# Optimization experiments

Hardware: AMD Instinct MI355X
Metric: run time of the kernel (lower is better)

Reference implementation:

```python
import jax, jax.numpy as jnp
import numpy as np

B, S, D, H = 2, 2048, 2048, 16
DK = D // H
THETA = 10000.0


def setup_inputs() -> dict:
    key = jax.random.key(0)
    ks = jax.random.split(key, 5)
    scale = 0.02
    return {
        "x": jax.random.normal(ks[0], (B, S, D), dtype=jnp.float32),
        "W_Q": jax.random.normal(ks[1], (D, D), dtype=jnp.float32) * scale,
        "W_K": jax.random.normal(ks[2], (D, D), dtype=jnp.float32) * scale,
        "W_V": jax.random.normal(ks[3], (D, D), dtype=jnp.float32) * scale,
        "W_O": jax.random.normal(ks[4], (D, D), dtype=jnp.float32) * scale,
        "token_positions": jnp.arange(S, dtype=jnp.int32),
    }


def _rope(x, pos):
    # x: [B, S, H, DK]; pos: [S]. Interleaved-pair rotation (cs336 RoPE).
    half = DK // 2
    inv_freq = THETA ** (-(jnp.arange(half, dtype=jnp.float32) / half))  # [half]
    ang = pos.astype(jnp.float32)[:, None] * inv_freq[None, :]           # [S, half]
    cos = jnp.cos(ang)[None, :, None, :]                                 # [1,S,1,half]
    sin = jnp.sin(ang)[None, :, None, :]
    x1, x2 = x[..., ::2], x[..., 1::2]
    r1 = x1 * cos - x2 * sin
    r2 = x1 * sin + x2 * cos
    return jnp.stack([r1, r2], axis=-1).reshape(x.shape)


def reference(x, W_Q, W_K, W_V, W_O, token_positions):
    # QKV projections (Linear with no bias: y = x @ W^T)
    Q = (x @ W_Q.T).reshape(B, S, H, DK)
    K = (x @ W_K.T).reshape(B, S, H, DK)
    V = (x @ W_V.T).reshape(B, S, H, DK)
    Q = _rope(Q, token_positions)
    K = _rope(K, token_positions)
    scores = jnp.einsum("bqhd,bkhd->bhqk", Q, K) / jnp.sqrt(jnp.float32(DK))
    causal = jnp.tril(jnp.ones((S, S), dtype=bool))  # True = attend
    scores = jnp.where(causal[None, None], scores, -jnp.inf)
    attn = jax.nn.softmax(scores, axis=-1)
    out = jnp.einsum("bhqk,bkhd->bqhd", attn, V).reshape(B, S, D)
    return out @ W_O.T
```

## Files before the change

### kernel.cpp

```cpp
#include <hip/hip_runtime.h>
#include <hip/hip_bf16.h>
#include <cstdint>
#include <cstddef>

#define B_ 2
#define S_ 2048
#define D_ 2048
#define H_ 16
#define DK_ 128
#define M_ (B_*S_)

typedef __attribute__((ext_vector_type(8))) __bf16 bf16x8;
typedef __attribute__((ext_vector_type(4))) float f32x4;
typedef __attribute__((ext_vector_type(16))) float f32x16;

__device__ __forceinline__ unsigned short f2bf(float f) {
  union { float f; unsigned int u; } v; v.f = f;
  unsigned int r = (v.u + 0x7fffu + ((v.u >> 16) & 1u)) >> 16;
  return (unsigned short)r;
}
__device__ __forceinline__ float bf2f(unsigned short b) {
  union { unsigned int u; float f; } v; v.u = ((unsigned int)b) << 16;
  return v.f;
}

__device__ __forceinline__ void gld16(const void* g, void* l) {
  __builtin_amdgcn_global_load_lds(
      (const __attribute__((address_space(1))) unsigned int*)g,
      (__attribute__((address_space(3))) unsigned int*)l, 16, 0, 0);
}

__global__ void cvt_all(const float* __restrict__ x,  const float* __restrict__ Wq,
                        const float* __restrict__ Wk, const float* __restrict__ Wv,
                        const float* __restrict__ Wo, unsigned short* __restrict__ dst) {
  size_t i = ((size_t)blockIdx.x * blockDim.x + threadIdx.x) * 4;
  const float* src;
  size_t off;
  if (i < ((size_t)M_ * D_)) {
    src = x; off = i;
  } else {
    size_t j = i - (size_t)M_ * D_;
    int w = (int)(j >> 22);
    off = j & ((1u << 22) - 1);
    src = (w == 0) ? Wq : (w == 1) ? Wk : (w == 2) ? Wv : Wo;
  }
  float4 v = *(const float4*)(src + off);
  dst[i+0] = f2bf(v.x); dst[i+1] = f2bf(v.y);
  dst[i+2] = f2bf(v.z); dst[i+3] = f2bf(v.w);
}

template<int WRITE_BF16>
__global__ __launch_bounds__(512, 2) void gemm8p(const unsigned short* __restrict__ A,
                                                 const unsigned short* __restrict__ W0,
                                                 const unsigned short* __restrict__ W1,
                                                 const unsigned short* __restrict__ W2,
                                                 void* __restrict__ C0, void* __restrict__ C1,
                                                 void* __restrict__ C2,
                                                 int M, int N, int K) {
  __shared__ unsigned short sA[2][2][256 * 32];
  __shared__ unsigned short sB[2][2][256 * 32];
  const int z = blockIdx.z;
  const unsigned short* Bt = (z == 0) ? W0 : (z == 1) ? W1 : W2;
  void* Cout = (z == 0) ? C0 : (z == 1) ? C1 : C2;

  const int tid  = threadIdx.x;
  const int lane = tid & 63;
  const int wid  = tid >> 6;
  const int wm = wid >> 2, wn = wid & 3;
  const int l16 = lane & 15, quad = lane >> 4;
  const int col16 = quad ^ ((lane >> 1) & 3);
  const int qk_log = (lane & 3) ^ ((lane >> 3) & 3);
  const int srow = lane >> 2;
  const int bm = blockIdx.y * 256, bn = blockIdx.x * 256;
  const int NT = K >> 6;

  f32x4 acc[8][4];
  #pragma unroll
  for (int i = 0; i < 8; ++i)
    #pragma unroll
    for (int j = 0; j < 4; ++j)
      acc[i][j] = (f32x4){0.f, 0.f, 0.f, 0.f};

  auto stage = [&](const unsigned short* __restrict__ g, int rowbase,
                   unsigned short* l, int t, int kh) {
    const unsigned short* src = g + (size_t)rowbase * K + t * 64 + kh * 32 + qk_log * 8;
    #pragma unroll
    for (int p = 0; p < 2; ++p) {
      const int i = wid * 2 + p;
      gld16(src + (size_t)(i * 16 + srow) * K, l + i * 512);
    }
  };

  stage(A,  bm, &sA[0][0][0], 0, 0);
  stage(Bt, bn, &sB[0][0][0], 0, 0);
  stage(A,  bm, &sA[0][1][0], 0, 1);
  stage(Bt, bn, &sB[0][1][0], 0, 1);
  stage(A,  bm, &sA[1][0][0], 1, 0);
  stage(Bt, bn, &sB[1][0][0], 1, 0);
  asm volatile("s_waitcnt vmcnt(4)" ::: "memory");
  __builtin_amdgcn_s_barrier();

  for (int t = 0; t < NT; ++t) {
    const int buf = t & 1;
    bf16x8 bfrag[4];
    #pragma unroll
    for (int ph = 0; ph < 4; ++ph) {
      const int ks = ph >> 1;
      const int mh = ph & 1;
      bf16x8 afrag[4];
      const unsigned short* aP = &sA[buf][ks][0] +
          (size_t)((wm * 128 + mh * 64 + l16) * 4 + col16) * 8;
      #pragma unroll
      for (int mf = 0; mf < 4; ++mf)
        afrag[mf] = *(const bf16x8*)(aP + mf * 512);
      if (mh == 0) {
        const unsigned short* bP = &sB[buf][ks][0] +
            (size_t)((wn * 64 + l16) * 4 + col16) * 8;
        #pragma unroll
        for (int nf = 0; nf < 4; ++nf)
          bfrag[nf] = *(const bf16x8*)(bP + nf * 512);
      }
      if (ph == 0)      { if (t + 1 < NT) stage(A,  bm, &sA[buf ^ 1][1][0], t + 1, 1); }
      else if (ph == 1) { if (t + 1 < NT) stage(Bt, bn, &sB[buf ^ 1][1][0], t + 1, 1); }
      else if (ph == 2) { if (t + 2 < NT) stage(A,  bm, &sA[buf][0][0],     t + 2, 0); }
      else              { if (t + 2 < NT) stage(Bt, bn, &sB[buf][0][0],     t + 2, 0); }

      __builtin_amdgcn_s_barrier();
      asm volatile("s_waitcnt lgkmcnt(0)" ::: "memory");
      __builtin_amdgcn_s_setprio(1);
      #pragma unroll
      for (int nf = 0; nf < 4; ++nf)
        #pragma unroll
        for (int mf = 0; mf < 4; ++mf)
          acc[mh * 4 + mf][nf] = __builtin_amdgcn_mfma_f32_16x16x32_bf16(
              afrag[mf], bfrag[nf], acc[mh * 4 + mf][nf], 0, 0, 0);
      __builtin_amdgcn_s_setprio(0);
      if (ph == 3) {
        if (t + 2 < NT) asm volatile("s_waitcnt vmcnt(4)" ::: "memory");
        else            asm volatile("s_waitcnt vmcnt(0)" ::: "memory");
      }
      __builtin_amdgcn_s_barrier();
    }
  }

  #pragma unroll
  for (int mf = 0; mf < 8; ++mf) {
    const int row = bm + wm * 128 + mf * 16 + quad * 4;
    #pragma unroll
    for (int nf = 0; nf < 4; ++nf) {
      const int col = bn + wn * 64 + nf * 16 + l16;
      #pragma unroll
      for (int r = 0; r < 4; ++r) {
        if (WRITE_BF16)
          ((unsigned short*)Cout)[(size_t)(row + r) * N + col] = f2bf(acc[mf][nf][r]);
        else
          ((float*)Cout)[(size_t)(row + r) * N + col] = acc[mf][nf][r];
      }
    }
  }
}

template<int WRITE_BF16>
__global__ __launch_bounds__(256) void gemm_bt(const unsigned short* __restrict__ A,
                                               const unsigned short* __restrict__ W0,
                                               const unsigned short* __restrict__ W1,
                                               const unsigned short* __restrict__ W2,
                                               void* __restrict__ C0, void* __restrict__ C1,
                                               void* __restrict__ C2,
                                               int M, int N, int K) {
  __shared__ unsigned short sA[128 * 32];
  __shared__ unsigned short sB[128 * 32];
  const int z = blockIdx.z;
  const unsigned short* Bt = (z == 0) ? W0 : (z == 1) ? W1 : W2;
  void* Cout = (z == 0) ? C0 : (z == 1) ? C1 : C2;

  const int tid  = threadIdx.x;
  const int lane = tid & 63;
  const int wid  = tid >> 6;
  const int wm = wid >> 1, wn = wid & 1;
  const int quad = lane >> 4, l16 = lane & 15;
  const int bm = blockIdx.y * 128, bn = blockIdx.x * 128;
  const int srow = lane >> 2;
  const int scol = (lane & 3) * 8;

  f32x4 acc[4][4];
  #pragma unroll
  for (int i = 0; i < 4; ++i)
    #pragma unroll
    for (int j = 0; j < 4; ++j)
      acc[i][j] = (f32x4){0.f, 0.f, 0.f, 0.f};

  for (int k0 = 0; k0 < K; k0 += 32) {
    __syncthreads();
    #pragma unroll
    for (int p = 0; p < 2; ++p) {
      int row = p * 64 + wid * 16;
      gld16(A  + (size_t)(bm + row + srow) * K + k0 + scol, sA + row * 32);
      gld16(Bt + (size_t)(bn + row + srow) * K + k0 + scol, sB + row * 32);
    }
    __syncthreads();

    bf16x8 af[4], bfr[4];
    #pragma unroll
    for (int i = 0; i < 4; ++i)
      af[i] = *(const bf16x8*)(sA + (wm * 64 + i * 16 + l16) * 32 + quad * 8);
    #pragma unroll
    for (int j = 0; j < 4; ++j)
      bfr[j] = *(const bf16x8*)(sB + (wn * 64 + j * 16 + l16) * 32 + quad * 8);
    #pragma unroll
    for (int i = 0; i < 4; ++i)
      #pragma unroll
      for (int j = 0; j < 4; ++j)
        acc[i][j] = __builtin_amdgcn_mfma_f32_16x16x32_bf16(af[i], bfr[j], acc[i][j], 0, 0, 0);
  }

  #pragma unroll
  for (int i = 0; i < 4; ++i) {
    int row = bm + wm * 64 + i * 16 + quad * 4;
    #pragma unroll
    for (int j = 0; j < 4; ++j) {
      int col = bn + wn * 64 + j * 16 + l16;
      #pragma unroll
      for (int r = 0; r < 4; ++r) {
        if (WRITE_BF16)
          ((unsigned short*)Cout)[(size_t)(row + r) * N + col] = f2bf(acc[i][j][r]);
        else
          ((float*)Cout)[(size_t)(row + r) * N + col] = acc[i][j][r];
      }
    }
  }
}

__global__ void rope_kernel(unsigned short* __restrict__ Q, unsigned short* __restrict__ K,
                            const int* __restrict__ pos) {
  int idx = blockIdx.x * blockDim.x + threadIdx.x;
  int i = idx & 63;
  int h = (idx >> 6) & (H_ - 1);
  int s = (idx >> 10) & (S_ - 1);
  int b = idx >> 21;
  float p = (float)pos[s];
  float inv = expf(-(float)i * (9.210340371976184f / 64.0f));
  float ang = p * inv;
  float sn, cs;
  sincosf(ang, &sn, &cs);
  size_t base = (((size_t)b * S_ + s) * D_) + (size_t)h * DK_ + 2 * i;
  float x1 = bf2f(Q[base]), x2 = bf2f(Q[base + 1]);
  Q[base]     = f2bf(x1 * cs - x2 * sn);
  Q[base + 1] = f2bf(x1 * sn + x2 * cs);
  x1 = bf2f(K[base]); x2 = bf2f(K[base + 1]);
  K[base]     = f2bf(x1 * cs - x2 * sn);
  K[base + 1] = f2bf(x1 * sn + x2 * cs);
}

__global__ __launch_bounds__(256) void transpose_bf16(const unsigned short* __restrict__ src,
                                                      unsigned short* __restrict__ dst) {
  __shared__ unsigned short sT[64 * 64];
  const int b = blockIdx.y;
  const int tx = blockIdx.x & 31, ty = blockIdx.x >> 5;
  const size_t base = (size_t)b * 2048 * 2048;
  const int m0 = ty * 64, c0 = tx * 64;
  const int tid = threadIdx.x;
  #pragma unroll
  for (int c = 0; c < 2; ++c) {
    int idx = tid + c * 256;
    int row = idx >> 3;
    int chk = idx & 7;
    uint4 v = *(const uint4*)(src + base + (size_t)(m0 + row) * 2048 + c0 + chk * 8);
    *(uint4*)(sT + row * 64 + ((chk ^ (row & 7)) * 8)) = v;
  }
  __syncthreads();
  #pragma unroll
  for (int c = 0; c < 2; ++c) {
    int idx = tid + c * 256;
    int orow = idx >> 3;
    int ocol = (idx & 7) * 8;
    unsigned short tmp[8];
    #pragma unroll
    for (int j = 0; j < 8; ++j) {
      int lr = ocol + j;
      int lc = orow;
      tmp[j] = sT[lr * 64 + (((lc >> 3) ^ (lr & 7)) * 8) + (lc & 7)];
    }
    *(uint4*)(dst + base + (size_t)(c0 + orow) * 2048 + m0 + ocol) = *(const uint4*)tmp;
  }
}

__global__ __launch_bounds__(256, 2) void flash_attn(const unsigned short* __restrict__ Q,
                                                     const unsigned short* __restrict__ K,
                                                     const unsigned short* __restrict__ VT,
                                                     unsigned short* __restrict__ O) {
  __shared__ unsigned short sK[2][64 * 128];
  __shared__ unsigned short sVT[2][128 * 64];
  __shared__ unsigned short sP[4][32 * 64];

  const int tid = threadIdx.x, lane = tid & 63, wid = tid >> 6;
  const int half = lane >> 5, l32 = lane & 31;
  const int qi = 15 - (blockIdx.x & 15);
  const int bh = blockIdx.x >> 4;
  const int h = bh & (H_ - 1), b = bh >> 4;
  const int qw = qi * 128 + wid * 32;
  const size_t qkbase = ((size_t)b * S_) * D_ + (size_t)h * DK_;
  const unsigned short* Qg = Q + qkbase;
  const unsigned short* Kg = K + qkbase;
  const unsigned short* VTg = VT + (size_t)bh * DK_ * S_;
  unsigned short* Og = O + qkbase;
  unsigned short* sPw = sP[wid];

  const int kKeySub = lane >> 4;
  const int kPhys   = lane & 15;
  const int vFeatSub = lane >> 3;
  const int vPhys    = lane & 7;

  bf16x8 qf[8];
  #pragma unroll
  for (int ks = 0; ks < 8; ++ks)
    qf[ks] = *(const bf16x8*)(Qg + (size_t)(qw + l32) * D_ + ks * 16 + half * 8);

  union { unsigned short u[8]; bf16x8 v; } onesu;
  #pragma unroll
  for (int j2 = 0; j2 < 8; ++j2) onesu.u[j2] = 0x3F80;
  const bf16x8 ones = onesu.v;

  f32x16 Oacc[4];
  #pragma unroll
  for (int ft = 0; ft < 4; ++ft)
    #pragma unroll
    for (int r = 0; r < 16; ++r) Oacc[ft][r] = 0.f;
  f32x16 l_acc;
  #pragma unroll
  for (int r = 0; r < 16; ++r) l_acc[r] = 0.f;
  const float scale = 0.08838834764831845f;

  const int nkb = 2 * (qi + 1);

  auto stage = [&](int kb) {
    const int k0 = kb * 64;
    unsigned short* bK = sK[kb & 1];
    unsigned short* bV = sVT[kb & 1];
    #pragma unroll
    for (int p = 0; p < 4; ++p) {
      int issue = wid * 4 + p;
      int key = issue * 4 + kKeySub;
      int logiK = (kPhys & 8) | ((kPhys ^ key) & 7);
      gld16(Kg + (size_t)(k0 + key) * D_ + logiK * 8, bK + issue * 512);
      int feat = issue * 8 + vFeatSub;
      int logiV = vPhys ^ (feat & 7);
      gld16(VTg + (size_t)feat * S_ + k0 + logiV * 8, bV + issue * 512);
    }
  };

  stage(0);

  for (int kb = 0; kb < nkb; ++kb) {
    __syncthreads();
    if (kb + 1 < nkb) stage(kb + 1);

    const int k0 = kb * 64;
    if (k0 > qw + 31) continue;

    const unsigned short* bK = sK[kb & 1];
    const unsigned short* bV = sVT[kb & 1];

    f32x16 sc[2];
    #pragma unroll
    for (int t = 0; t < 2; ++t)
      #pragma unroll
      for (int r = 0; r < 16; ++r) sc[t][r] = 0.f;
    #pragma unroll
    for (int ks = 0; ks < 8; ++ks) {
      const int logi = ks * 2 + half;
      #pragma unroll
      for (int t = 0; t < 2; ++t) {
        const int key = t * 32 + l32;
        const int phys = (logi & 8) | ((logi ^ key) & 7);
        bf16x8 kf = *(const bf16x8*)(bK + key * 128 + phys * 8);
        sc[t] = __builtin_amdgcn_mfma_f32_32x32x16_bf16(qf[ks], kf, sc[t], 0, 0, 0);
      }
    }

    const bool diag = (k0 + 63 > qw);
    #pragma unroll
    for (int t = 0; t < 2; ++t) {
      const int col = t * 32 + l32;
      const int keyg = k0 + col;
      #pragma unroll
      for (int r = 0; r < 16; ++r) {
        const int rl = (r & 3) + 8 * (r >> 2) + 4 * half;
        float v = sc[t][r] * scale;
        if (diag && (keyg > qw + rl)) v = -1e30f;
        sPw[rl * 64 + (((col >> 3) ^ (rl & 7)) * 8) + (col & 7)] = f2bf(__expf(v));
      }
    }

    #pragma unroll
    for (int ksp = 0; ksp < 4; ++ksp) {
      const int logi = ksp * 2 + half;
      bf16x8 pf = *(const bf16x8*)(sPw + l32 * 64 + ((logi ^ (l32 & 7)) * 8));
      l_acc = __builtin_amdgcn_mfma_f32_32x32x16_bf16(pf, ones, l_acc, 0, 0, 0);
      #pragma unroll
      for (int ft = 0; ft < 4; ++ft) {
        const int feat = ft * 32 + l32;
        const int phys = logi ^ (feat & 7);
        bf16x8 vf = *(const bf16x8*)(bV + feat * 64 + phys * 8);
        Oacc[ft] = __builtin_amdgcn_mfma_f32_32x32x16_bf16(pf, vf, Oacc[ft], 0, 0, 0);
      }
    }
  }

  #pragma unroll
  for (int ft = 0; ft < 4; ++ft) {
    const int feat = ft * 32 + l32;
    #pragma unroll
    for (int r = 0; r < 16; ++r) {
      const int rl = (r & 3) + 8 * (r >> 2) + 4 * half;
      Og[(size_t)(qw + rl) * D_ + feat] = f2bf(Oacc[ft][r] / l_acc[r]);
    }
  }
}

extern "C" void kernel_launch(void* const* d_in, const int* in_sizes, int n_in,
                              void* d_out, int out_size, void* d_ws, size_t ws_size,
                              hipStream_t stream) {
  const float* x  = (const float*)d_in[0];
  const float* Wq = (const float*)d_in[1];
  const float* Wk = (const float*)d_in[2];
  const float* Wv = (const float*)d_in[3];
  const float* Wo = (const float*)d_in[4];
  const int*  pos = (const int*)d_in[5];
  float* out = (float*)d_out;

  char* ws = (char*)d_ws;
  size_t off = 0;
  auto alloc = [&](size_t bytes) { void* p = ws + off; off += (bytes + 255) & ~255ULL; return p; };
  const size_t nx = (size_t)M_ * D_;
  const size_t nw = (size_t)D_ * D_;
  unsigned short* xb  = (unsigned short*)alloc(nx * 2);
  unsigned short* wqb = (unsigned short*)alloc(nw * 2);
  unsigned short* wkb = (unsigned short*)alloc(nw * 2);
  unsigned short* wvb = (unsigned short*)alloc(nw * 2);
  unsigned short* wob = (unsigned short*)alloc(nw * 2);
  unsigned short* Qb  = (unsigned short*)alloc(nx * 2);
  unsigned short* Kb  = (unsigned short*)alloc(nx * 2);
  unsigned short* Vb  = (unsigned short*)alloc(nx * 2);
  unsigned short* AOb = xb;
  unsigned short* VTb = wqb;

  hipLaunchKernelGGL(cvt_all, dim3((nx + 4 * nw) / 1024), dim3(256), 0, stream,
                     x, Wq, Wk, Wv, Wo, xb);

  hipLaunchKernelGGL((gemm8p<1>), dim3(D_ / 256, M_ / 256, 3), dim3(512), 0, stream,
                     xb, wqb, wkb, wvb, (void*)Qb, (void*)Kb, (void*)Vb, M_, D_, D_);

  hipLaunchKernelGGL(rope_kernel, dim3((B_ * S_ * H_ * 64) / 256), dim3(256), 0, stream, Qb, Kb, pos);

  hipLaunchKernelGGL(transpose_bf16, dim3(1024, 2), dim3(256), 0, stream, Vb, VTb);

  hipLaunchKernelGGL(flash_attn, dim3(B_ * H_ * (S_ / 128)), dim3(256), 0, stream, Qb, Kb, VTb, AOb);

  hipLaunchKernelGGL((gemm_bt<0>), dim3(D_ / 128, M_ / 128, 1), dim3(256), 0, stream,
                     AOb, wob, wob, wob, (void*)out, (void*)out, (void*)out, M_, D_, D_);
}
```

Measured before the change: 438.5 us.

## Rebalance QKV GEMM grid with smaller V tiles, vectorize RoPE, prioritize attention MFMA

The 3-way QKV GEMM grid of 384 blocks of 256x256 tiles is replaced by a 1D grid of 512 blocks. Q and K keep 256x256 tiles, while V uses 128x256 tiles so the grid spreads better across the 256 CUs and the tail wave shrinks. The RoPE kernel now uses fast intrinsics and packed 32-bit loads and stores. The flash attention MFMA sections are also wrapped in s_setprio. The V tiles have lower arithmetic intensity, and the fast sincos may lose some precision at large angles.

```diff
diff --git a/kernel.cpp b/kernel.cpp
--- a/kernel.cpp
+++ b/kernel.cpp
@@ -49,112 +49,194 @@
   dst[i+2] = f2bf(v.z); dst[i+3] = f2bf(v.w);
 }
 
-template<int WRITE_BF16>
-__global__ __launch_bounds__(512, 2) void gemm8p(const unsigned short* __restrict__ A,
-                                                 const unsigned short* __restrict__ W0,
-                                                 const unsigned short* __restrict__ W1,
-                                                 const unsigned short* __restrict__ W2,
-                                                 void* __restrict__ C0, void* __restrict__ C1,
-                                                 void* __restrict__ C2,
-                                                 int M, int N, int K) {
+__global__ __launch_bounds__(512, 2) void gemm_qkv(const unsigned short* __restrict__ A,
+                                                   const unsigned short* __restrict__ W0,
+                                                   const unsigned short* __restrict__ W1,
+                                                   const unsigned short* __restrict__ W2,
+                                                   unsigned short* __restrict__ C0,
+                                                   unsigned short* __restrict__ C1,
+                                                   unsigned short* __restrict__ C2,
+                                                   int M, int N, int K) {
   __shared__ unsigned short sA[2][2][256 * 32];
   __shared__ unsigned short sB[2][2][256 * 32];
-  const int z = blockIdx.z;
-  const unsigned short* Bt = (z == 0) ? W0 : (z == 1) ? W1 : W2;
-  void* Cout = (z == 0) ? C0 : (z == 1) ? C1 : C2;
-
+  const int id   = blockIdx.x;
   const int tid  = threadIdx.x;
   const int lane = tid & 63;
   const int wid  = tid >> 6;
-  const int wm = wid >> 2, wn = wid & 3;
   const int l16 = lane & 15, quad = lane >> 4;
   const int col16 = quad ^ ((lane >> 1) & 3);
   const int qk_log = (lane & 3) ^ ((lane >> 3) & 3);
   const int srow = lane >> 2;
-  const int bm = blockIdx.y * 256, bn = blockIdx.x * 256;
   const int NT = K >> 6;
 
-  f32x4 acc[8][4];
-  #pragma unroll
-  for (int i = 0; i < 8; ++i)
-    #pragma unroll
-    for (int j = 0; j < 4; ++j)
-      acc[i][j] = (f32x4){0.f, 0.f, 0.f, 0.f};
-
-  auto stage = [&](const unsigned short* __restrict__ g, int rowbase,
-                   unsigned short* l, int t, int kh) {
-    const unsigned short* src = g + (size_t)rowbase * K + t * 64 + kh * 32 + qk_log * 8;
-    #pragma unroll
-    for (int p = 0; p < 2; ++p) {
-      const int i = wid * 2 + p;
-      gld16(src + (size_t)(i * 16 + srow) * K, l + i * 512);
-    }
-  };
-
-  stage(A,  bm, &sA[0][0][0], 0, 0);
-  stage(Bt, bn, &sB[0][0][0], 0, 0);
-  stage(A,  bm, &sA[0][1][0], 0, 1);
-  stage(Bt, bn, &sB[0][1][0], 0, 1);
-  stage(A,  bm, &sA[1][0][0], 1, 0);
-  stage(Bt, bn, &sB[1][0][0], 1, 0);
-  asm volatile("s_waitcnt vmcnt(4)" ::: "memory");
-  __builtin_amdgcn_s_barrier();
-
-  for (int t = 0; t < NT; ++t) {
-    const int buf = t & 1;
-    bf16x8 bfrag[4];
-    #pragma unroll
-    for (int ph = 0; ph < 4; ++ph) {
-      const int ks = ph >> 1;
-      const int mh = ph & 1;
-      bf16x8 afrag[4];
-      const unsigned short* aP = &sA[buf][ks][0] +
-          (size_t)((wm * 128 + mh * 64 + l16) * 4 + col16) * 8;
-      #pragma unroll
-      for (int mf = 0; mf < 4; ++mf)
-        afrag[mf] = *(const bf16x8*)(aP + mf * 512);
-      if (mh == 0) {
-        const unsigned short* bP = &sB[buf][ks][0] +
+  if (id < 256) {
+    const int z = id >> 7, r = id & 127;
+    const unsigned short* Bt = z ? W1 : W0;
+    unsigned short* Cout = z ? C1 : C0;
+    const int bm = (r >> 3) * 256, bn = (r & 7) * 256;
+    const int wm = wid >> 2, wn = wid & 3;
+
+    f32x4 acc[8][4];
+    #pragma unroll
+    for (int i = 0; i < 8; ++i)
+      #pragma unroll
+      for (int j = 0; j < 4; ++j)
+        acc[i][j] = (f32x4){0.f, 0.f, 0.f, 0.f};
+
+    auto stage = [&](const unsigned short* __restrict__ g, int rowbase,
+                     unsigned short* l, int t, int kh) {
+      const unsigned short* src = g + (size_t)rowbase * K + t * 64 + kh * 32 + qk_log * 8;
+      #pragma unroll
+      for (int p = 0; p < 2; ++p) {
+        const int i = wid * 2 + p;
+        gld16(src + (size_t)(i * 16 + srow) * K, l + i * 512);
+      }
+    };
+
+    stage(A,  bm, &sA[0][0][0], 0, 0);
+    stage(Bt, bn, &sB[0][0][0], 0, 0);
+    stage(A,  bm, &sA[0][1][0], 0, 1);
+    stage(Bt, bn, &sB[0][1][0], 0, 1);
+    stage(A,  bm, &sA[1][0][0], 1, 0);
+    stage(Bt, bn, &sB[1][0][0], 1, 0);
+    asm volatile("s_waitcnt vmcnt(4)" ::: "memory");
+    __builtin_amdgcn_s_barrier();
+
+    for (int t = 0; t < NT; ++t) {
+      const int buf = t & 1;
+      bf16x8 bfrag[4];
+      #pragma unroll
+      for (int ph = 0; ph < 4; ++ph) {
+        const int ks = ph >> 1;
+        const int mh = ph & 1;
+        bf16x8 afrag[4];
+        const unsigned short* aP = &sA[buf][ks][0] +
+            (size_t)((wm * 128 + mh * 64 + l16) * 4 + col16) * 8;
+        #pragma unroll
+        for (int mf = 0; mf < 4; ++mf)
+          afrag[mf] = *(const bf16x8*)(aP + mf * 512);
+        if (mh == 0) {
+          const unsigned short* bP = &sB[buf][ks][0] +
+              (size_t)((wn * 64 + l16) * 4 + col16) * 8;
+          #pragma unroll
+          for (int nf = 0; nf < 4; ++nf)
+            bfrag[nf] = *(const bf16x8*)(bP + nf * 512);
+        }
+        if (ph == 0)      { if (t + 1 < NT) stage(A,  bm, &sA[buf ^ 1][1][0], t + 1, 1); }
+        else if (ph == 1) { if (t + 1 < NT) stage(Bt, bn, &sB[buf ^ 1][1][0], t + 1, 1); }
+        else if (ph == 2) { if (t + 2 < NT) stage(A,  bm, &sA[buf][0][0],     t + 2, 0); }
+        else              { if (t + 2 < NT) stage(Bt, bn, &sB[buf][0][0],     t + 2, 0); }
+
+        __builtin_amdgcn_s_barrier();
+        asm volatile("s_waitcnt lgkmcnt(0)" ::: "memory");
+        __builtin_amdgcn_s_setprio(1);
+        #pragma unroll
+        for (int nf = 0; nf < 4; ++nf)
+          #pragma unroll
+          for (int mf = 0; mf < 4; ++mf)
+            acc[mh * 4 + mf][nf] = __builtin_amdgcn_mfma_f32_16x16x32_bf16(
+                afrag[mf], bfrag[nf], acc[mh * 4 + mf][nf], 0, 0, 0);
+        __builtin_amdgcn_s_setprio(0);
+        if (ph == 3) {
+          if (t + 2 < NT) asm volatile("s_waitcnt vmcnt(4)" ::: "memory");
+          else            asm volatile("s_waitcnt vmcnt(0)" ::: "memory");
+        }
+        __builtin_amdgcn_s_barrier();
+      }
+    }
+
+    #pragma unroll
+    for (int mf = 0; mf < 8; ++mf) {
+      const int row = bm + wm * 128 + mf * 16 + quad * 4;
+      #pragma unroll
+      for (int nf = 0; nf < 4; ++nf) {
+        const int col = bn + wn * 64 + nf * 16 + l16;
+        #pragma unroll
+        for (int rr = 0; rr < 4; ++rr)
+          Cout[(size_t)(row + rr) * N + col] = f2bf(acc[mf][nf][rr]);
+      }
+    }
+  } else {
+    const int r = id - 256;
+    const unsigned short* Bt = W2;
+    unsigned short* Cout = C2;
+    const int bm = (r >> 3) * 128, bn = (r & 7) * 256;
+    const int wm = wid >> 2, wn = wid & 3;
+
+    f32x4 acc[4][4];
+    #pragma unroll
+    for (int i = 0; i < 4; ++i)
+      #pragma unroll
+      for (int j = 0; j < 4; ++j)
+        acc[i][j] = (f32x4){0.f, 0.f, 0.f, 0.f};
+
+    auto stageB = [&](unsigned short* l, int t, int kh) {
+      const unsigned short* src = Bt + (size_t)bn * K + t * 64 + kh * 32 + qk_log * 8;
+      #pragma unroll
+      for (int p = 0; p < 2; ++p) {
+        const int i = wid * 2 + p;
+        gld16(src + (size_t)(i * 16 + srow) * K, l + i * 512);
+      }
+    };
+    auto stageA = [&](unsigned short* l, int t, int kh) {
+      const unsigned short* src = A + (size_t)bm * K + t * 64 + kh * 32 + qk_log * 8;
+      gld16(src + (size_t)(wid * 16 + srow) * K, l + wid * 512);
+    };
+
+    stageA(&sA[0][0][0], 0, 0); stageB(&sB[0][0][0], 0, 0);
+    stageA(&sA[0][1][0], 0, 1); stageB(&sB[0][1][0], 0, 1);
+    stageA(&sA[1][0][0], 1, 0); stageB(&sB[1][0][0], 1, 0);
+    asm volatile("s_waitcnt vmcnt(3)" ::: "memory");
+    __builtin_amdgcn_s_barrier();
+
+    for (int t = 0; t < NT; ++t) {
+      const int buf = t & 1;
+      #pragma unroll
+      for (int ph = 0; ph < 2; ++ph) {
+        bf16x8 afrag[4], bfrag[4];
+        const unsigned short* aP = &sA[buf][ph][0] +
+            (size_t)((wm * 64 + l16) * 4 + col16) * 8;
+        #pragma unroll
+        for (int mf = 0; mf < 4; ++mf)
+          afrag[mf] = *(const bf16x8*)(aP + mf * 512);
+        const unsigned short* bP = &sB[buf][ph][0] +
             (size_t)((wn * 64 + l16) * 4 + col16) * 8;
         #pragma unroll
         for (int nf = 0; nf < 4; ++nf)
           bfrag[nf] = *(const bf16x8*)(bP + nf * 512);
-      }
-      if (ph == 0)      { if (t + 1 < NT) stage(A,  bm, &sA[buf ^ 1][1][0], t + 1, 1); }
-      else if (ph == 1) { if (t + 1 < NT) stage(Bt, bn, &sB[buf ^ 1][1][0], t + 1, 1); }
-      else if (ph == 2) { if (t + 2 < NT) stage(A,  bm, &sA[buf][0][0],     t + 2, 0); }
-      else              { if (t + 2 < NT) stage(Bt, bn, &sB[buf][0][0],     t + 2, 0); }
-
-      __builtin_amdgcn_s_barrier();
-      asm volatile("s_waitcnt lgkmcnt(0)" ::: "memory");
-      __builtin_amdgcn_s_setprio(1);
-      #pragma unroll
-      for (int nf = 0; nf < 4; ++nf)
-        #pragma unroll
-        for (int mf = 0; mf < 4; ++mf)
-          acc[mh * 4 + mf][nf] = __builtin_amdgcn_mfma_f32_16x16x32_bf16(
-              afrag[mf], bfrag[nf], acc[mh * 4 + mf][nf], 0, 0, 0);
-      __builtin_amdgcn_s_setprio(0);
-      if (ph == 3) {
-        if (t + 2 < NT) asm volatile("s_waitcnt vmcnt(4)" ::: "memory");
-        else            asm volatile("s_waitcnt vmcnt(0)" ::: "memory");
-      }
-      __builtin_amdgcn_s_barrier();
-    }
-  }
-
-  #pragma unroll
-  for (int mf = 0; mf < 8; ++mf) {
-    const int row = bm + wm * 128 + mf * 16 + quad * 4;
-    #pragma unroll
-    for (int nf = 0; nf < 4; ++nf) {
-      const int col = bn + wn * 64 + nf * 16 + l16;
-      #pragma unroll
-      for (int r = 0; r < 4; ++r) {
-        if (WRITE_BF16)
-          ((unsigned short*)Cout)[(size_t)(row + r) * N + col] = f2bf(acc[mf][nf][r]);
-        else
-          ((float*)Cout)[(size_t)(row + r) * N + col] = acc[mf][nf][r];
+
+        if (ph == 0) { if (t + 1 < NT) { stageA(&sA[buf ^ 1][1][0], t + 1, 1);
+                                         stageB(&sB[buf ^ 1][1][0], t + 1, 1); } }
+        else         { if (t + 2 < NT) { stageA(&sA[buf][0][0], t + 2, 0);
+                                         stageB(&sB[buf][0][0], t + 2, 0); } }
+
+        __builtin_amdgcn_s_barrier();
+        asm volatile("s_waitcnt lgkmcnt(0)" ::: "memory");
+        __builtin_amdgcn_s_setprio(1);
+        #pragma unroll
+        for (int nf = 0; nf < 4; ++nf)
+          #pragma unroll
+          for (int mf = 0; mf < 4; ++mf)
+            acc[mf][nf] = __builtin_amdgcn_mfma_f32_16x16x32_bf16(
+                afrag[mf], bfrag[nf], acc[mf][nf], 0, 0, 0);
+        __builtin_amdgcn_s_setprio(0);
+        if (ph == 1) {
+          if (t + 2 < NT) asm volatile("s_waitcnt vmcnt(3)" ::: "memory");
+          else            asm volatile("s_waitcnt vmcnt(0)" ::: "memory");
+        }
+        __builtin_amdgcn_s_barrier();
+      }
+    }
+
+    #pragma unroll
+    for (int mf = 0; mf < 4; ++mf) {
+      const int row = bm + wm * 64 + mf * 16 + quad * 4;
+      #pragma unroll
+      for (int nf = 0; nf < 4; ++nf) {
+        const int col = bn + wn * 64 + nf * 16 + l16;
+        #pragma unroll
+        for (int rr = 0; rr < 4; ++rr)
+          Cout[(size_t)(row + rr) * N + col] = f2bf(acc[mf][nf][rr]);
       }
     }
   }
@@ -239,17 +321,19 @@
   int s = (idx >> 10) & (S_ - 1);
   int b = idx >> 21;
   float p = (float)pos[s];
-  float inv = expf(-(float)i * (9.210340371976184f / 64.0f));
+  float inv = __expf(-(float)i * (9.210340371976184f / 64.0f));
   float ang = p * inv;
   float sn, cs;
-  sincosf(ang, &sn, &cs);
+  __sincosf(ang, &sn, &cs);
   size_t base = (((size_t)b * S_ + s) * D_) + (size_t)h * DK_ + 2 * i;
-  float x1 = bf2f(Q[base]), x2 = bf2f(Q[base + 1]);
-  Q[base]     = f2bf(x1 * cs - x2 * sn);
-  Q[base + 1] = f2bf(x1 * sn + x2 * cs);
-  x1 = bf2f(K[base]); x2 = bf2f(K[base + 1]);
-  K[base]     = f2bf(x1 * cs - x2 * sn);
-  K[base + 1] = f2bf(x1 * sn + x2 * cs);
+  unsigned int q2 = *(const unsigned int*)(Q + base);
+  float x1 = bf2f((unsigned short)(q2 & 0xffffu)), x2 = bf2f((unsigned short)(q2 >> 16));
+  unsigned int lo = f2bf(x1 * cs - x2 * sn), hi = f2bf(x1 * sn + x2 * cs);
+  *(unsigned int*)(Q + base) = lo | (hi << 16);
+  unsigned int k2 = *(const unsigned int*)(K + base);
+  x1 = bf2f((unsigned short)(k2 & 0xffffu)); x2 = bf2f((unsigned short)(k2 >> 16));
+  lo = f2bf(x1 * cs - x2 * sn); hi = f2bf(x1 * sn + x2 * cs);
+  *(unsigned int*)(K + base) = lo | (hi << 16);
 }
 
 __global__ __launch_bounds__(256) void transpose_bf16(const unsigned short* __restrict__ src,
@@ -366,6 +450,7 @@
     for (int t = 0; t < 2; ++t)
       #pragma unroll
       for (int r = 0; r < 16; ++r) sc[t][r] = 0.f;
+    __builtin_amdgcn_s_setprio(1);
     #pragma unroll
     for (int ks = 0; ks < 8; ++ks) {
       const int logi = ks * 2 + half;
@@ -377,6 +462,7 @@
         sc[t] = __builtin_amdgcn_mfma_f32_32x32x16_bf16(qf[ks], kf, sc[t], 0, 0, 0);
       }
     }
+    __builtin_amdgcn_s_setprio(0);
 
     const bool diag = (k0 + 63 > qw);
     #pragma unroll
@@ -392,6 +478,7 @@
       }
     }
 
+    __builtin_amdgcn_s_setprio(1);
     #pragma unroll
     for (int ksp = 0; ksp < 4; ++ksp) {
       const int logi = ksp * 2 + half;
@@ -405,6 +492,7 @@
         Oacc[ft] = __builtin_amdgcn_mfma_f32_32x32x16_bf16(pf, vf, Oacc[ft], 0, 0, 0);
       }
     }
+    __builtin_amdgcn_s_setprio(0);
   }
 
   #pragma unroll
@@ -448,8 +536,8 @@
   hipLaunchKernelGGL(cvt_all, dim3((nx + 4 * nw) / 1024), dim3(256), 0, stream,
                      x, Wq, Wk, Wv, Wo, xb);
 
-  hipLaunchKernelGGL((gemm8p<1>), dim3(D_ / 256, M_ / 256, 3), dim3(512), 0, stream,
-                     xb, wqb, wkb, wvb, (void*)Qb, (void*)Kb, (void*)Vb, M_, D_, D_);
+  hipLaunchKernelGGL(gemm_qkv, dim3(512), dim3(512), 0, stream,
+                     xb, wqb, wkb, wvb, Qb, Kb, Vb, M_, D_, D_);
 
   hipLaunchKernelGGL(rope_kernel, dim3((B_ * S_ * H_ * 64) / 256), dim3(256), 0, stream, Qb, Kb, pos);
 
```

New measurement: 415.5 us. 5.3% less time.
